# Kernel tuning notes

Hardware: AMD Instinct MI355X
Metric: run time of the kernel (lower is better)

## Reference

```python
import jax, jax.numpy as jnp
import numpy as np

T, B, E, H = 512, 32, 512, 2048

def setup_inputs() -> dict:
    key = jax.random.key(0)
    k1, k2, k3 = jax.random.split(key, 3)
    sent = jax.random.normal(k1, (T, B, E), dtype=jnp.float32)
    lengths = jax.random.randint(k2, (B,), 1, T + 1)  # unused by the math (pack is never applied)
    # Linear(E, 3H) params (PyTorch default-ish init scale)
    W = jax.random.normal(k3, (3 * H, E), dtype=jnp.float32) * (1.0 / np.sqrt(E))
    b = jnp.zeros((3 * H,), dtype=jnp.float32)
    return {"sent": sent, "lengths": lengths, "W": W, "b": b}

def reference(sent, lengths, W, b):
    # sent: (T, B, E) time-major. Single QRNN layer, window=1, output_gate=True, zoneout=0.
    Y = jnp.einsum('tbe,he->tbh', sent, W) + b          # (T, B, 3H)
    Z, F, O = jnp.split(Y, 3, axis=-1)
    Z = jnp.tanh(Z)
    F = jax.nn.sigmoid(F)
    O = jax.nn.sigmoid(O)

    # forget-mult recurrence: c_t = f_t * z_t + (1 - f_t) * c_{t-1}, c_0 = 0
    def step(c, zf):
        z, f = zf
        c = f * z + (1.0 - f) * c
        return c, c
    c0 = jnp.zeros_like(Z[0])                            # (B, H)
    _, C = jax.lax.scan(step, c0, (Z, F))                # (T, B, H)

    Hseq = O * C                                         # QRNN output (T, B, H)
    embeds = jnp.max(Hseq, axis=0)                       # torch.max(sent_output, 0)[0] -> (B, H)
    return embeds
```

## Files before the change

kernel.cpp:

```cpp
#include <hip/hip_runtime.h>
#include <stdint.h>

#define TT 512
#define BB 32
#define EE 512
#define HH 2048

typedef __attribute__((ext_vector_type(8))) short short8;
typedef __attribute__((ext_vector_type(4))) float f32x4;

#define XROW 528
#define XBUF (16 * XROW)

static __device__ __forceinline__ float fast_exp(float x) {
    return __builtin_amdgcn_exp2f(x * 1.44269504f);
}
static __device__ __forceinline__ float fast_rcp(float x) {
    return __builtin_amdgcn_rcpf(x);
}

static __device__ __forceinline__ unsigned cvtpk_bf16(float lo, float hi) {
    unsigned r;
    asm("v_cvt_pk_bf16_f32 %0, %1, %2" : "=v"(r) : "v"(lo), "v"(hi));
    return r;
}

static __device__ __forceinline__ void load_lds16(const unsigned short* g, unsigned short* l) {
    __builtin_amdgcn_global_load_lds(
        (const __attribute__((address_space(1))) unsigned int*)(uintptr_t)g,
        (__attribute__((address_space(3))) unsigned int*)(uintptr_t)l,
        16, 0, 0);
}

__launch_bounds__(256, 8)
__global__ void convert_inputs(const float* __restrict__ X,
                               const float* __restrict__ W,
                               unsigned short* __restrict__ Xb,
                               unsigned short* __restrict__ Wb) {
    const int bid = blockIdx.x;
    const float* src;
    unsigned short* dst;
    size_t base;
    if (bid < 2048) { src = X; dst = Xb; base = (size_t)bid * 4096; }
    else            { src = W; dst = Wb; base = (size_t)(bid - 2048) * 4096; }
    size_t j = base + (size_t)threadIdx.x * 16;

    float4 v0 = *(const float4*)(src + j);
    float4 v1 = *(const float4*)(src + j + 4);
    float4 v2 = *(const float4*)(src + j + 8);
    float4 v3 = *(const float4*)(src + j + 12);
    union { short8 s; unsigned u[4]; } o0, o1;
    o0.u[0] = cvtpk_bf16(v0.x, v0.y);
    o0.u[1] = cvtpk_bf16(v0.z, v0.w);
    o0.u[2] = cvtpk_bf16(v1.x, v1.y);
    o0.u[3] = cvtpk_bf16(v1.z, v1.w);
    o1.u[0] = cvtpk_bf16(v2.x, v2.y);
    o1.u[1] = cvtpk_bf16(v2.z, v2.w);
    o1.u[2] = cvtpk_bf16(v3.x, v3.y);
    o1.u[3] = cvtpk_bf16(v3.z, v3.w);
    *(short8*)(dst + j)     = o0.s;
    *(short8*)(dst + j + 8) = o1.s;
}

__launch_bounds__(256, 3)
__global__ void qrnn_fused(const unsigned short* __restrict__ Xb,
                           const unsigned short* __restrict__ Wb,
                           const float* __restrict__ bias,
                           float* __restrict__ out)
{
    __shared__ unsigned short xlds[2 * XBUF];
    __shared__ float exch[2][64][12];

    const int tid  = threadIdx.x;
    const int wv   = tid >> 6;
    const int lane = tid & 63;
    const int q    = lane >> 4;
    const int c    = lane & 15;

    const int id   = blockIdx.x;
    const int xcd  = id & 7;
    const int slot = id >> 3;
    const int b    = xcd * 4 + (slot >> 7);
    const int hgrp = slot & 127;
    const int h    = hgrp * 16 + c;

    const int  scanwv = slot & 3;
    const bool isScan = (wv == scanwv);
    const int  gsel   = (wv < scanwv) ? wv : wv - 1;

    float carry = 0.0f;
    float vmax  = -1e30f;
    float b0 = 0.f, b1 = 0.f, b2 = 0.f;

    short8 wg[16];
    if (!isScan) {
        const unsigned short* wr = Wb + ((size_t)gsel * HH + h) * EE;
#pragma unroll
        for (int k = 0; k < 16; ++k)
            wg[k] = *(const short8*)(wr + k * 32 + q * 8);
#pragma unroll
        for (int k = 0; k < 16; ++k)
            asm volatile("" : "+a"(wg[k]));
    } else {
        b0 = bias[h];
        b1 = bias[HH + h];
        b2 = bias[2 * HH + h];
    }

    const unsigned short* g0 = Xb + ((size_t)(wv * 4) * BB + b) * EE + lane * 8;
    unsigned short* l0 = &xlds[(wv * 4) * XROW];

    auto stage = [&](int n, int slt) {
        const unsigned short* g = g0 + (size_t)n * (16 * BB * EE);
        unsigned short* l = l0 + slt * XBUF;
#pragma unroll
        for (int i = 0; i < 4; ++i)
            load_lds16(g + (size_t)i * (BB * EE), l + i * XROW);
    };

    auto do_tail = [&](f32x4 az, f32x4 af, f32x4 ao) {
        float aa[4], mm[4], oo[4];
#pragma unroll
        for (int r = 0; r < 4; ++r) {
            float e2 = fast_exp(2.0f * az[r]);
            float z  = 1.0f - 2.0f * fast_rcp(e2 + 1.0f);
            float f  = fast_rcp(1.0f + fast_exp(-af[r]));
            float o  = fast_rcp(1.0f + fast_exp(-ao[r]));
            aa[r] = f * z;
            mm[r] = 1.0f - f;
            oo[r] = o;
        }

        float A = aa[0], M = mm[0];
#pragma unroll
        for (int r = 1; r < 4; ++r) { A = aa[r] + mm[r] * A; M = mm[r] * M; }

        float Ap = __shfl_up(A, 16, 64), Mp = __shfl_up(M, 16, 64);
        if (q >= 1) { A = A + M * Ap; M = M * Mp; }
        Ap = __shfl_up(A, 32, 64); Mp = __shfl_up(M, 32, 64);
        if (q >= 2) { A = A + M * Ap; M = M * Mp; }
        float Ae = __shfl_up(A, 16, 64), Me = __shfl_up(M, 16, 64);
        if (q == 0) { Ae = 0.0f; Me = 1.0f; }
        float cc = Ae + Me * carry;

#pragma unroll
        for (int r = 0; r < 4; ++r) {
            cc = aa[r] + mm[r] * cc;
            vmax = fmaxf(vmax, oo[r] * cc);
        }

        float cend = A + M * carry;
        carry = __shfl(cend, 48 + c, 64);
    };

    stage(0, 0);
    __syncthreads();

    for (int ch = 0; ch < 32; ++ch) {
        const int buf = ch & 1;
        if (ch < 31) stage(ch + 1, buf ^ 1);

        if (!isScan) {
            const unsigned short* Abase = &xlds[buf * XBUF + c * XROW + q * 8];
            f32x4 ac0 = {0.f, 0.f, 0.f, 0.f};
            f32x4 ac1 = {0.f, 0.f, 0.f, 0.f};
#pragma unroll
            for (int half = 0; half < 2; ++half) {
                short8 a[8];
#pragma unroll
                for (int j = 0; j < 8; ++j)
                    a[j] = *(const short8*)(Abase + (half * 8 + j) * 32);
#pragma unroll
                for (int j = 0; j < 8; ++j) {
                    if (j & 1)
                        ac1 = __builtin_amdgcn_mfma_f32_16x16x32_bf16(a[j], wg[half * 8 + j], ac1, 0, 0, 0);
                    else
                        ac0 = __builtin_amdgcn_mfma_f32_16x16x32_bf16(a[j], wg[half * 8 + j], ac0, 0, 0, 0);
                }
            }
            f32x4 ac = ac0 + ac1;
            *(f32x4*)(&exch[ch & 1][lane][gsel * 4]) = ac;
        } else {
            if (ch > 0) {
                const float* e = &exch[(ch - 1) & 1][lane][0];
                f32x4 az = *(const f32x4*)(e);
                f32x4 af = *(const f32x4*)(e + 4);
                f32x4 ao = *(const f32x4*)(e + 8);
#pragma unroll
                for (int r = 0; r < 4; ++r) { az[r] += b0; af[r] += b1; ao[r] += b2; }
                do_tail(az, af, ao);
            }
        }

        __syncthreads();
    }

    if (isScan) {
        const float* e = &exch[31 & 1][lane][0];
        f32x4 az = *(const f32x4*)(e);
        f32x4 af = *(const f32x4*)(e + 4);
        f32x4 ao = *(const f32x4*)(e + 8);
#pragma unroll
        for (int r = 0; r < 4; ++r) { az[r] += b0; af[r] += b1; ao[r] += b2; }
        do_tail(az, af, ao);

        vmax = fmaxf(vmax, __shfl_xor(vmax, 16, 64));
        vmax = fmaxf(vmax, __shfl_xor(vmax, 32, 64));
        if (q == 0) out[(size_t)b * HH + h] = vmax;
    }
}

extern "C" void kernel_launch(void* const* d_in, const int* in_sizes, int n_in,
                              void* d_out, int out_size, void* d_ws, size_t ws_size,
                              hipStream_t stream) {
    const float* sent = (const float*)d_in[0];
    const float* W    = (const float*)d_in[2];
    const float* bias = (const float*)d_in[3];
    float* out        = (float*)d_out;

    const int nX = TT * BB * EE;
    unsigned short* Xb = (unsigned short*)d_ws;
    unsigned short* Wb = Xb + nX;

    convert_inputs<<<2816, 256, 0, stream>>>(sent, W, Xb, Wb);

    dim3 grid(4096);
    qrnn_fused<<<grid, 256, 0, stream>>>(Xb, Wb, bias, out);
}
```

Measured before the change: 237.8 us.

## Split time axis into two halves per block with deferred carry-fixup scan

Each block now runs 512 threads as two independent 4-wave teams, each handling half of the time sequence (16 chunks each), with the scan wave storing per-chunk affine summaries (A, M) and per-step O-scaled partials in registers. After both halves finish, one wave does a serial scan over the 32 chunk summaries to compute entry carries, and the scan waves then apply those carries to their stored partials to take the max. This halves the serial chain length per block and doubles in-flight work, at the cost of twice the LDS staging buffers, many registers for the stored partials, and extra barriers.

```diff
diff --git a/kernel.cpp b/kernel.cpp
--- a/kernel.cpp
+++ b/kernel.cpp
@@ -62,20 +62,25 @@
     *(short8*)(dst + j + 8) = o1.s;
 }
 
-__launch_bounds__(256, 3)
+__launch_bounds__(512, 2)
 __global__ void qrnn_fused(const unsigned short* __restrict__ Xb,
                            const unsigned short* __restrict__ Wb,
                            const float* __restrict__ bias,
                            float* __restrict__ out)
 {
-    __shared__ unsigned short xlds[2 * XBUF];
-    __shared__ float exch[2][64][12];
+    __shared__ unsigned short xlds[4 * XBUF];
+    __shared__ float exch[2][2][64][12];
+    __shared__ float summ[32][16][2];
+    __shared__ float entry[32][16];
+    __shared__ float rmax[2][16];
 
     const int tid  = threadIdx.x;
     const int wv   = tid >> 6;
     const int lane = tid & 63;
     const int q    = lane >> 4;
     const int c    = lane & 15;
+    const int th   = wv >> 2;
+    const int role = wv & 3;
 
     const int id   = blockIdx.x;
     const int xcd  = id & 7;
@@ -84,129 +89,161 @@
     const int hgrp = slot & 127;
     const int h    = hgrp * 16 + c;
 
-    const int  scanwv = slot & 3;
-    const bool isScan = (wv == scanwv);
-    const int  gsel   = (wv < scanwv) ? wv : wv - 1;
-
-    float carry = 0.0f;
-    float vmax  = -1e30f;
-    float b0 = 0.f, b1 = 0.f, b2 = 0.f;
-
-    short8 wg[16];
-    if (!isScan) {
-        const unsigned short* wr = Wb + ((size_t)gsel * HH + h) * EE;
-#pragma unroll
-        for (int k = 0; k < 16; ++k)
-            wg[k] = *(const short8*)(wr + k * 32 + q * 8);
-#pragma unroll
-        for (int k = 0; k < 16; ++k)
-            asm volatile("" : "+a"(wg[k]));
-    } else {
-        b0 = bias[h];
-        b1 = bias[HH + h];
-        b2 = bias[2 * HH + h];
-    }
-
-    const unsigned short* g0 = Xb + ((size_t)(wv * 4) * BB + b) * EE + lane * 8;
-    unsigned short* l0 = &xlds[(wv * 4) * XROW];
-
-    auto stage = [&](int n, int slt) {
-        const unsigned short* g = g0 + (size_t)n * (16 * BB * EE);
-        unsigned short* l = l0 + slt * XBUF;
+    const unsigned short* g0 =
+        Xb + ((size_t)(th * 256 + role * 4) * BB + b) * EE + lane * 8;
+    unsigned short* l0 = &xlds[th * 2 * XBUF] + role * 4 * XROW;
+
+    auto stage = [&](int n, int buf) {
+        const unsigned short* g = g0 + (size_t)n * 16 * BB * EE;
+        unsigned short* l = l0 + buf * XBUF;
 #pragma unroll
         for (int i = 0; i < 4; ++i)
             load_lds16(g + (size_t)i * (BB * EE), l + i * XROW);
     };
 
-    auto do_tail = [&](f32x4 az, f32x4 af, f32x4 ao) {
-        float aa[4], mm[4], oo[4];
-#pragma unroll
-        for (int r = 0; r < 4; ++r) {
-            float e2 = fast_exp(2.0f * az[r]);
-            float z  = 1.0f - 2.0f * fast_rcp(e2 + 1.0f);
-            float f  = fast_rcp(1.0f + fast_exp(-af[r]));
-            float o  = fast_rcp(1.0f + fast_exp(-ao[r]));
-            aa[r] = f * z;
-            mm[r] = 1.0f - f;
-            oo[r] = o;
-        }
-
-        float A = aa[0], M = mm[0];
-#pragma unroll
-        for (int r = 1; r < 4; ++r) { A = aa[r] + mm[r] * A; M = mm[r] * M; }
-
-        float Ap = __shfl_up(A, 16, 64), Mp = __shfl_up(M, 16, 64);
-        if (q >= 1) { A = A + M * Ap; M = M * Mp; }
-        Ap = __shfl_up(A, 32, 64); Mp = __shfl_up(M, 32, 64);
-        if (q >= 2) { A = A + M * Ap; M = M * Mp; }
-        float Ae = __shfl_up(A, 16, 64), Me = __shfl_up(M, 16, 64);
-        if (q == 0) { Ae = 0.0f; Me = 1.0f; }
-        float cc = Ae + Me * carry;
-
-#pragma unroll
-        for (int r = 0; r < 4; ++r) {
-            cc = aa[r] + mm[r] * cc;
-            vmax = fmaxf(vmax, oo[r] * cc);
-        }
-
-        float cend = A + M * carry;
-        carry = __shfl(cend, 48 + c, 64);
-    };
-
-    stage(0, 0);
-    __syncthreads();
-
-    for (int ch = 0; ch < 32; ++ch) {
-        const int buf = ch & 1;
-        if (ch < 31) stage(ch + 1, buf ^ 1);
-
-        if (!isScan) {
-            const unsigned short* Abase = &xlds[buf * XBUF + c * XROW + q * 8];
+    if (role < 3) {
+        short8 wg[16];
+        {
+            const unsigned short* wr = Wb + ((size_t)role * HH + h) * EE;
+#pragma unroll
+            for (int k = 0; k < 16; ++k)
+                wg[k] = *(const short8*)(wr + k * 32 + q * 8);
+#pragma unroll
+            for (int k = 0; k < 16; ++k)
+                asm volatile("" : "+a"(wg[k]));
+        }
+
+        stage(0, 0);
+        __syncthreads();
+
+        for (int ch = 0; ch < 16; ++ch) {
+            const int buf = ch & 1;
+            if (ch < 15) stage(ch + 1, buf ^ 1);
+
+            const unsigned short* Ab =
+                &xlds[(th * 2 + buf) * XBUF] + c * XROW + q * 8;
+            short8 a[16];
+#pragma unroll
+            for (int k = 0; k < 16; ++k)
+                a[k] = *(const short8*)(Ab + k * 32);
+
             f32x4 ac0 = {0.f, 0.f, 0.f, 0.f};
             f32x4 ac1 = {0.f, 0.f, 0.f, 0.f};
 #pragma unroll
-            for (int half = 0; half < 2; ++half) {
-                short8 a[8];
-#pragma unroll
-                for (int j = 0; j < 8; ++j)
-                    a[j] = *(const short8*)(Abase + (half * 8 + j) * 32);
-#pragma unroll
-                for (int j = 0; j < 8; ++j) {
-                    if (j & 1)
-                        ac1 = __builtin_amdgcn_mfma_f32_16x16x32_bf16(a[j], wg[half * 8 + j], ac1, 0, 0, 0);
-                    else
-                        ac0 = __builtin_amdgcn_mfma_f32_16x16x32_bf16(a[j], wg[half * 8 + j], ac0, 0, 0, 0);
-                }
+            for (int k = 0; k < 16; k += 2) {
+                ac0 = __builtin_amdgcn_mfma_f32_16x16x32_bf16(a[k],     wg[k],     ac0, 0, 0, 0);
+                ac1 = __builtin_amdgcn_mfma_f32_16x16x32_bf16(a[k + 1], wg[k + 1], ac1, 0, 0, 0);
             }
             f32x4 ac = ac0 + ac1;
-            *(f32x4*)(&exch[ch & 1][lane][gsel * 4]) = ac;
-        } else {
-            if (ch > 0) {
-                const float* e = &exch[(ch - 1) & 1][lane][0];
-                f32x4 az = *(const f32x4*)(e);
-                f32x4 af = *(const f32x4*)(e + 4);
-                f32x4 ao = *(const f32x4*)(e + 8);
-#pragma unroll
-                for (int r = 0; r < 4; ++r) { az[r] += b0; af[r] += b1; ao[r] += b2; }
-                do_tail(az, af, ao);
-            }
-        }
-
-        __syncthreads();
-    }
-
-    if (isScan) {
-        const float* e = &exch[31 & 1][lane][0];
-        f32x4 az = *(const f32x4*)(e);
-        f32x4 af = *(const f32x4*)(e + 4);
-        f32x4 ao = *(const f32x4*)(e + 8);
-#pragma unroll
-        for (int r = 0; r < 4; ++r) { az[r] += b0; af[r] += b1; ao[r] += b2; }
-        do_tail(az, af, ao);
-
+            *(f32x4*)(&exch[buf][th][lane][role * 4]) = ac;
+
+            __syncthreads();
+        }
+
+        __syncthreads();
+
+        if (wv == 0 && lane < 16) {
+            float As[32], Ms[32];
+#pragma unroll
+            for (int n = 0; n < 32; ++n) {
+                As[n] = summ[n][lane][0];
+                Ms[n] = summ[n][lane][1];
+            }
+            float cr = 0.0f;
+#pragma unroll
+            for (int n = 0; n < 32; ++n) {
+                entry[n][lane] = cr;
+                cr = As[n] + Ms[n] * cr;
+            }
+        }
+        __syncthreads();
+        __syncthreads();
+
+        if (wv == 0 && lane < 16)
+            out[(size_t)b * HH + hgrp * 16 + lane] =
+                fmaxf(rmax[0][lane], rmax[1][lane]);
+    } else {
+        const float b0 = bias[h];
+        const float b1 = bias[HH + h];
+        const float b2 = bias[2 * HH + h];
+
+        float pOA[16][4], pOM[16][4];
+        float vmax = -1e30f;
+
+        auto tailwork = [&](int ct, int sb) {
+            const float* e = &exch[sb][th][lane][0];
+            f32x4 az = *(const f32x4*)(e);
+            f32x4 af = *(const f32x4*)(e + 4);
+            f32x4 ao = *(const f32x4*)(e + 8);
+
+            float aa[4], mm[4], oo[4];
+#pragma unroll
+            for (int r = 0; r < 4; ++r) {
+                float zz = az[r] + b0;
+                float ff = af[r] + b1;
+                float ov = ao[r] + b2;
+                float e2 = fast_exp(2.0f * zz);
+                float z  = 1.0f - 2.0f * fast_rcp(e2 + 1.0f);
+                float f  = fast_rcp(1.0f + fast_exp(-ff));
+                float o  = fast_rcp(1.0f + fast_exp(-ov));
+                aa[r] = f * z;
+                mm[r] = 1.0f - f;
+                oo[r] = o;
+            }
+
+            float A = aa[0], M = mm[0];
+#pragma unroll
+            for (int r = 1; r < 4; ++r) { A = aa[r] + mm[r] * A; M = mm[r] * M; }
+
+            float Ap = __shfl_up(A, 16, 64), Mp = __shfl_up(M, 16, 64);
+            if (q >= 1) { A = A + M * Ap; M = M * Mp; }
+            Ap = __shfl_up(A, 32, 64); Mp = __shfl_up(M, 32, 64);
+            if (q >= 2) { A = A + M * Ap; M = M * Mp; }
+            float Ae = __shfl_up(A, 16, 64), Me = __shfl_up(M, 16, 64);
+            if (q == 0) { Ae = 0.0f; Me = 1.0f; }
+
+            float cc = Ae, MM = Me;
+#pragma unroll
+            for (int r = 0; r < 4; ++r) {
+                cc = aa[r] + mm[r] * cc;
+                MM = mm[r] * MM;
+                pOA[ct][r] = oo[r] * cc;
+                pOM[ct][r] = oo[r] * MM;
+            }
+
+            if (lane >= 48) {
+                summ[th * 16 + ct][c][0] = A;
+                summ[th * 16 + ct][c][1] = M;
+            }
+        };
+
+        stage(0, 0);
+        __syncthreads();
+
+#pragma unroll
+        for (int ch = 0; ch < 16; ++ch) {
+            const int buf = ch & 1;
+            if (ch < 15) stage(ch + 1, buf ^ 1);
+            if (ch > 0) tailwork(ch - 1, buf ^ 1);
+            __syncthreads();
+        }
+        tailwork(15, 1);
+
+        __syncthreads();
+        __syncthreads();
+
+#pragma unroll
+        for (int n = 0; n < 16; ++n) {
+            float ec = entry[th * 16 + n][c];
+#pragma unroll
+            for (int r = 0; r < 4; ++r)
+                vmax = fmaxf(vmax, pOA[n][r] + pOM[n][r] * ec);
+        }
         vmax = fmaxf(vmax, __shfl_xor(vmax, 16, 64));
         vmax = fmaxf(vmax, __shfl_xor(vmax, 32, 64));
-        if (q == 0) out[(size_t)b * HH + h] = vmax;
+        if (q == 0) rmax[th][c] = vmax;
+
+        __syncthreads();
     }
 }
 
@@ -225,5 +262,5 @@
     convert_inputs<<<2816, 256, 0, stream>>>(sent, W, Xb, Wb);
 
     dim3 grid(4096);
-    qrnn_fused<<<grid, 256, 0, stream>>>(Xb, Wb, bias, out);
-}
+    qrnn_fused<<<grid, 512, 0, stream>>>(Xb, Wb, bias, out);
+}
```

Result: slower. 374.7 us (+57.5%).
